# Performance work log

Hardware: AMD Instinct MI355X
Metric: run time of the kernel (lower is better)

The kernel has to match this reference:

```python
import jax, jax.numpy as jnp
import numpy as np

B, T_INIT, IN, H, OUT, GEN = 128, 50, 171, 1024, 171, 100


def setup_inputs() -> dict:
    key = jax.random.key(0)
    ks = jax.random.split(key, 20)
    s = 1.0 / np.sqrt(H)  # torch LSTMCell/Linear init scale

    def u(k, shape):
        return jax.random.uniform(k, shape, jnp.float32, -s, s)

    return {
        "initial_seq": jax.random.normal(ks[0], (B, T_INIT, IN), jnp.float32),
        "generate_frames_number": GEN,
        "w_ih1": u(ks[1], (4 * H, IN)), "w_hh1": u(ks[2], (4 * H, H)),
        "b_ih1": u(ks[3], (4 * H,)), "b_hh1": u(ks[4], (4 * H,)),
        "w_ih2": u(ks[5], (4 * H, H)), "w_hh2": u(ks[6], (4 * H, H)),
        "b_ih2": u(ks[7], (4 * H,)), "b_hh2": u(ks[8], (4 * H,)),
        "w_ih3": u(ks[9], (4 * H, H)), "w_hh3": u(ks[10], (4 * H, H)),
        "b_ih3": u(ks[11], (4 * H,)), "b_hh3": u(ks[12], (4 * H,)),
        "w_dec": u(ks[13], (OUT, H)), "b_dec": u(ks[14], (OUT,)),
    }


def _lstm_cell(x, h, c, w_ih, w_hh, b_ih, b_hh):
    # PyTorch LSTMCell: gates ordered (i, f, g, o)
    gates = x @ w_ih.T + b_ih + h @ w_hh.T + b_hh
    i, f, g, o = jnp.split(gates, 4, axis=-1)
    c_new = jax.nn.sigmoid(f) * c + jax.nn.sigmoid(i) * jnp.tanh(g)
    h_new = jax.nn.sigmoid(o) * jnp.tanh(c_new)
    return h_new, c_new


def reference(initial_seq, generate_frames_number,
              w_ih1, w_hh1, b_ih1, b_hh1,
              w_ih2, w_hh2, b_ih2, b_hh2,
              w_ih3, w_hh3, b_ih3, b_hh3,
              w_dec, b_dec):
    batch = initial_seq.shape[0]
    hid = w_hh1.shape[1]
    z = jnp.zeros((batch, hid), initial_seq.dtype)

    def step(carry, in_frame):
        h0, c0, h1, c1, h2, c2 = carry
        h0, c0 = _lstm_cell(in_frame, h0, c0, w_ih1, w_hh1, b_ih1, b_hh1)
        h1, c1 = _lstm_cell(h0, h1, c1, w_ih2, w_hh2, b_ih2, b_hh2)
        h2, c2 = _lstm_cell(h1, h2, c2, w_ih3, w_hh3, b_ih3, b_hh3)
        out = h2 @ w_dec.T + b_dec
        return (h0, c0, h1, c1, h2, c2), out

    # Conditioning phase: feed ground-truth frames; only states (and last out) matter.
    carry = (z, z, z, z, z, z)
    def cond_step(cs, frame):
        carry, _ = cs
        carry, out = step(carry, frame)
        return (carry, out), None
    (carry, current_frame), _ = jax.lax.scan(
        cond_step, (carry, jnp.zeros((batch, w_dec.shape[0]), initial_seq.dtype)),
        jnp.swapaxes(initial_seq, 0, 1))  # [T_init, B, IN]

    def gen_step(cs, _):
        carry, frame = cs
        carry, out = step(carry, frame)
        return (carry, out), out
    _, outs = jax.lax.scan(gen_step, (carry, current_frame), None,
                           length=generate_frames_number)
    return jnp.swapaxes(outs, 0, 1)  # [B, GEN, OUT]
```

## Files before the change

### kernel.cpp

```cpp
#include <hip/hip_runtime.h>

typedef __attribute__((ext_vector_type(8))) short short8;
typedef __attribute__((ext_vector_type(8))) _Float16 f16x8;
typedef __attribute__((ext_vector_type(4))) float f32x4;

#define GENF 100
#define TCOND 50
#define BATCH 128
#define HID 1024
#define INP 171
#define INPAD 192
#define OUTN 171
#define OUTPAD 176
#define SPLITS 4
#define TILES 64
#define PSTR ((size_t)BATCH * 4096)

static __device__ __forceinline__ unsigned short f2h(float f) {
  _Float16 h = (_Float16)f;
  return __builtin_bit_cast(unsigned short, h);
}
static __device__ __forceinline__ float h2f(unsigned short s) {
  return (float)__builtin_bit_cast(_Float16, s);
}
static __device__ __forceinline__ f16x8 ld8(const unsigned short* p) {
  short8 v = *reinterpret_cast<const short8*>(p);
  return __builtin_bit_cast(f16x8, v);
}
static __device__ __forceinline__ float sigm(float x) { return 1.f / (1.f + __expf(-x)); }

__global__ __launch_bounds__(256) void lstm_gemm_k(
    const unsigned short* __restrict__ xh_, const unsigned short* __restrict__ xl_,
    int ldx, int xc,
    const unsigned short* __restrict__ hh_, const unsigned short* __restrict__ hl_,
    const unsigned short* __restrict__ wP, int NKW, int nkr,
    const float* __restrict__ bias,
    float* __restrict__ c,
    unsigned short* __restrict__ ohh, unsigned short* __restrict__ ohl,
    unsigned short* __restrict__ histh, unsigned short* __restrict__ histl,
    float* __restrict__ partials, unsigned* __restrict__ counters, unsigned tgt)
{
  __shared__ __align__(16) char smem[98304];
  const int t = threadIdx.x;
  const int lane = t & 63, wv = t >> 6;
  const int nt = blockIdx.x & (TILES - 1), sp = blockIdx.x >> 6;
  const int n0 = nt * 64 + wv * 16;
  const int nit = NKW / SPLITS;
  const int beg = sp * nit;
  const int ns = nit >> 1;

  const int r_row = lane & 15, kg = lane >> 4;
  const int rslot = kg ^ (r_row & 3);
  const int srow = t >> 2;
  const unsigned short* wlane = wP + ((size_t)nt * NKW) * 2048
                                + (wv * 16 + r_row) * 32 + kg * 8;

  auto stage1 = [&](char* dst, int ck) {
    if (ck >= nkr) ck = 0;
    const unsigned short *sh, *sl;
    int ld, k0;
    if (ck < xc) { sh = xh_; sl = xl_; ld = ldx; k0 = ck * 32; }
    else { sh = hh_; sl = hl_; ld = HID; k0 = (ck - xc) * 32; }
#pragma unroll
    for (int j = 0; j < 2; ++j) {
      int rowp = j * 64 + srow;
      int slot = (t & 3) ^ (rowp & 3);
      const unsigned short* gh = sh + (size_t)rowp * ld + k0 + slot * 8;
      const unsigned short* gl = sl + (size_t)rowp * ld + k0 + slot * 8;
      char* dh = dst + j * 4096 + wv * 1024;
      char* dl = dst + 8192 + j * 4096 + wv * 1024;
      __builtin_amdgcn_global_load_lds((const __attribute__((address_space(1))) void*)gh,
                                       (__attribute__((address_space(3))) void*)dh, 16, 0, 0);
      __builtin_amdgcn_global_load_lds((const __attribute__((address_space(1))) void*)gl,
                                       (__attribute__((address_space(3))) void*)dl, 16, 0, 0);
    }
  };

  f32x4 zz = {0.f, 0.f, 0.f, 0.f};
  f32x4 acc[8] = {zz, zz, zz, zz, zz, zz, zz, zz};

  char* bA = smem;
  char* bB = smem + 32768;
  char* bC = smem + 65536;

  stage1(bA, beg);
  stage1(bA + 16384, beg + 1);
  f16x8 b0h0 = ld8(wlane + (size_t)(beg + 0) * 2048);
  f16x8 b0h1 = ld8(wlane + (size_t)(beg + 1) * 2048);
  __builtin_amdgcn_sched_barrier(0);
  stage1(bB, beg + 2);
  stage1(bB + 16384, beg + 3);
  f16x8 b1h0 = ld8(wlane + (size_t)(beg + 2) * 2048);
  f16x8 b1h1 = ld8(wlane + (size_t)(beg + 3) * 2048);
  __builtin_amdgcn_sched_barrier(0);

  for (int i = 0; i < ns; ++i) {
    int ck = beg + 2 * i + 4;
    if (ck >= beg + nit) ck = beg;
    stage1(bC, ck);
    stage1(bC + 16384, ck + 1);
    f16x8 b2h0 = ld8(wlane + (size_t)ck * 2048);
    f16x8 b2h1 = ld8(wlane + (size_t)(ck + 1) * 2048);
    __builtin_amdgcn_sched_barrier(0);

    asm volatile("s_waitcnt vmcnt(20)" ::: "memory");
    __builtin_amdgcn_s_barrier();
    __builtin_amdgcn_sched_barrier(0);

#pragma unroll
    for (int ch = 0; ch < 2; ++ch) {
      f16x8 ah[8], al[8];
#pragma unroll
      for (int rg = 0; rg < 8; ++rg) {
        int ro = ch * 16384 + (rg * 16 + r_row) * 64 + rslot * 16;
        ah[rg] = *reinterpret_cast<const f16x8*>(bA + ro);
        al[rg] = *reinterpret_cast<const f16x8*>(bA + ro + 8192);
      }
      f16x8 BH = ch ? b0h1 : b0h0;
#pragma unroll
      for (int rg = 0; rg < 8; ++rg)
        acc[rg] = __builtin_amdgcn_mfma_f32_16x16x32_f16(ah[rg], BH, acc[rg], 0, 0, 0);
#pragma unroll
      for (int rg = 0; rg < 8; ++rg)
        acc[rg] = __builtin_amdgcn_mfma_f32_16x16x32_f16(al[rg], BH, acc[rg], 0, 0, 0);
    }
    __builtin_amdgcn_sched_barrier(0);
    __builtin_amdgcn_s_barrier();

    char* tmp = bA; bA = bB; bB = bC; bC = tmp;
    b0h0 = b1h0; b0h1 = b1h1;
    b1h0 = b2h0; b1h1 = b2h1;
  }

  {
    float* pb = partials + (size_t)sp * PSTR;
    const int cn = n0 + r_row;
    const int mb = kg * 4;
#pragma unroll
    for (int rg = 0; rg < 8; ++rg)
#pragma unroll
      for (int r = 0; r < 4; ++r)
        pb[(size_t)(rg * 16 + mb + r) * 4096 + cn] = acc[rg][r];
  }

  __syncthreads();
  if (t == 0)
    __hip_atomic_fetch_add(&counters[nt], 1u, __ATOMIC_RELEASE, __HIP_MEMORY_SCOPE_AGENT);
  if (t == 0) {
    while (__hip_atomic_load(&counters[nt], __ATOMIC_RELAXED, __HIP_MEMORY_SCOPE_AGENT) < tgt)
      __builtin_amdgcn_s_sleep(2);
    (void)__hip_atomic_load(&counters[nt], __ATOMIC_ACQUIRE, __HIP_MEMORY_SCOPE_AGENT);
  }
  __syncthreads();

  const int fc = t & 15, fm = t >> 4;
  const int nh = nt * 16 + fc;
  const f32x4 bv = *reinterpret_cast<const f32x4*>(&bias[nh * 4]);
#pragma unroll
  for (int p = 0; p < 2; ++p) {
    int m = sp * 32 + p * 16 + fm;
    size_t gi0 = (size_t)m * 4096 + nh * 4;
    f32x4 s = *reinterpret_cast<const f32x4*>(&partials[gi0]);
#pragma unroll
    for (int q = 1; q < SPLITS; ++q)
      s += *reinterpret_cast<const f32x4*>(&partials[gi0 + (size_t)q * PSTR]);
    float gi = sigm(s[0] + bv[0]);
    float gf = sigm(s[1] + bv[1]);
    float gg = tanhf(s[2] + bv[2]);
    float go = sigm(s[3] + bv[3]);
    size_t sidx = (size_t)m * HID + nh;
    float cn2 = gf * c[sidx] + gi * gg;
    c[sidx] = cn2;
    float h = go * tanhf(cn2);
    unsigned short h16 = f2h(h);
    unsigned short l16 = f2h(h - h2f(h16));
    ohh[sidx] = h16;
    ohl[sidx] = l16;
    if (histh) { histh[sidx] = h16; histl[sidx] = l16; }
  }
}

__global__ __launch_bounds__(256) void decb_k(
    const unsigned short* __restrict__ histh, const unsigned short* __restrict__ histl,
    const unsigned short* __restrict__ wdh, const float* __restrict__ bd,
    float* __restrict__ outp)
{
  const int wave = threadIdx.x >> 6, lane = threadIdx.x & 63;
  const int n0 = ((int)blockIdx.x % 11) * 16;
  const int m0 = ((int)blockIdx.x / 11) * 16;
  const int row = lane & 15, kg = lane >> 4;
  f32x4 acc = {0.f, 0.f, 0.f, 0.f};
  const unsigned short* pah = histh + (size_t)(m0 + row) * HID + kg * 8 + wave * 256;
  const unsigned short* pal = histl + (size_t)(m0 + row) * HID + kg * 8 + wave * 256;
  const unsigned short* pbh = wdh + (size_t)(n0 + row) * HID + kg * 8 + wave * 256;
#pragma unroll
  for (int kk = 0; kk < 8; ++kk) {
    int off = kk * 32;
    f16x8 a1 = ld8(pah + off), a2 = ld8(pal + off);
    f16x8 b1 = ld8(pbh + off);
    acc = __builtin_amdgcn_mfma_f32_16x16x32_f16(a1, b1, acc, 0, 0, 0);
    acc = __builtin_amdgcn_mfma_f32_16x16x32_f16(a2, b1, acc, 0, 0, 0);
  }
  __shared__ f32x4 red[4][64];
  if (wave) red[wave][lane] = acc;
  __syncthreads();
  if (wave == 0) {
    acc += red[1][lane];
    acc += red[2][lane];
    acc += red[3][lane];
    const int col = lane & 15, rg = lane >> 4;
#pragma unroll
    for (int r = 0; r < 4; ++r) {
      int m = m0 + rg * 4 + r;
      int n = n0 + col;
      if (n < OUTN) {
        int tt = m >> 7, b = m & 127;
        outp[(size_t)b * (GENF * OUTN) + (size_t)tt * OUTN + n] = acc[r] + bd[n];
      }
    }
  }
}

__global__ void cvt_w_pack_k(const float* __restrict__ src, unsigned short* __restrict__ dst,
                             int C, int Cpad, int ck0, int NKW)
{
  int idx = blockIdx.x * 256 + threadIdx.x;
  if (idx >= 4096 * Cpad) return;
  int r = idx / Cpad, cc = idx - r * Cpad;
  float v = (cc < C) ? src[(size_t)r * C + cc] : 0.f;
  int rp = (r & 1023) * 4 + (r >> 10);
  int nt = rp >> 6, nc = rp & 63;
  int ck = ck0 + (cc >> 5), kk = cc & 31;
  dst[(((size_t)nt * NKW + ck) * 64 + nc) * 32 + kk] = f2h(v);
}

__global__ void cvt_plain_k(const float* __restrict__ src, unsigned short* __restrict__ w16,
                            int R, int C, int Rp, int Cp)
{
  int idx = blockIdx.x * 256 + threadIdx.x;
  if (idx >= Rp * Cp) return;
  int r = idx / Cp, c2 = idx - r * Cp;
  float v = (r < R && c2 < C) ? src[(size_t)r * C + c2] : 0.f;
  w16[idx] = f2h(v);
}

__global__ void cvt_wdt_k(const float* __restrict__ wdec, unsigned short* __restrict__ wdt)
{
  int idx = blockIdx.x * 256 + threadIdx.x;
  if (idx >= 1024 * 192) return;
  int k = idx / 192, j = idx - k * 192;
  float v = (j < OUTN) ? wdec[(size_t)j * HID + k] : 0.f;
  wdt[idx] = f2h(v);
}

__global__ __launch_bounds__(256) void weff_k(
    const unsigned short* __restrict__ wih, const unsigned short* __restrict__ wdt,
    unsigned short* __restrict__ W1g)
{
  const int wave = threadIdx.x >> 6, lane = threadIdx.x & 63;
  const int tile = blockIdx.x * 4 + wave;
  const int m0 = (tile >> 6) * 16;
  const int n0 = (tile & 63) * 16;
  const int row = lane & 15, kg = lane >> 4;
  f32x4 acc = {0.f, 0.f, 0.f, 0.f};
  const unsigned short* pa = wih + (size_t)(m0 + row) * 192 + kg * 8;
  const unsigned short* pb = wdt + (size_t)(n0 + row) * 192 + kg * 8;
#pragma unroll
  for (int kk = 0; kk < 6; ++kk) {
    int off = kk * 32;
    f16x8 a = ld8(pa + off);
    f16x8 b = ld8(pb + off);
    acc = __builtin_amdgcn_mfma_f32_16x16x32_f16(a, b, acc, 0, 0, 0);
  }
  const int col = lane & 15, rg = lane >> 4;
#pragma unroll
  for (int r = 0; r < 4; ++r) {
    int i = m0 + rg * 4 + r;
    int k2 = n0 + col;
    int rp = (i & 1023) * 4 + (i >> 10);
    int nt = rp >> 6, nc = rp & 63;
    int ck = k2 >> 5, kk2 = k2 & 31;
    W1g[(((size_t)nt * 64 + ck) * 64 + nc) * 32 + kk2] = f2h(acc[r]);
  }
}

__global__ void beff_k(const float* __restrict__ wih1, const float* __restrict__ bih,
                       const float* __restrict__ bhh, const float* __restrict__ bdec,
                       float* __restrict__ dst)
{
  int i = blockIdx.x * 256 + threadIdx.x;
  if (i >= 4096) return;
  float a = bih[i] + bhh[i];
  for (int j = 0; j < OUTN; ++j) a += wih1[(size_t)i * OUTN + j] * bdec[j];
  dst[(i & 1023) * 4 + (i >> 10)] = a;
}

__global__ void bias_perm_k(const float* __restrict__ a, const float* __restrict__ b,
                            float* __restrict__ dst)
{
  int i = blockIdx.x * 256 + threadIdx.x;
  if (i < 4096) dst[(i & 1023) * 4 + (i >> 10)] = a[i] + b[i];
}

__global__ void biaspad_k(const float* __restrict__ a, float* __restrict__ dst, int n, int np)
{
  int i = blockIdx.x * 256 + threadIdx.x;
  if (i < np) dst[i] = (i < n) ? a[i] : 0.f;
}

__global__ void xcond_k(const float* __restrict__ seq, unsigned short* __restrict__ xhi,
                        unsigned short* __restrict__ xlo)
{
  int idx = blockIdx.x * 256 + threadIdx.x;
  const int total = TCOND * BATCH * INPAD;
  if (idx >= total) return;
  int t = idx / (BATCH * INPAD);
  int rem = idx - t * (BATCH * INPAD);
  int b = rem / INPAD;
  int k = rem - b * INPAD;
  float v = (k < INP) ? seq[((size_t)b * TCOND + t) * INP + k] : 0.f;
  unsigned short h = f2h(v);
  xhi[idx] = h;
  xlo[idx] = f2h(v - h2f(h));
}

extern "C" void kernel_launch(void* const* d_in, const int* in_sizes, int n_in,
                              void* d_out, int out_size, void* d_ws, size_t ws_size,
                              hipStream_t stream)
{
  (void)in_sizes; (void)n_in; (void)out_size;
  const float* seq   = (const float*)d_in[0];
  const float* w_ih1 = (const float*)d_in[2];
  const float* w_hh1 = (const float*)d_in[3];
  const float* b_ih1 = (const float*)d_in[4];
  const float* b_hh1 = (const float*)d_in[5];
  const float* w_ih2 = (const float*)d_in[6];
  const float* w_hh2 = (const float*)d_in[7];
  const float* b_ih2 = (const float*)d_in[8];
  const float* b_hh2 = (const float*)d_in[9];
  const float* w_ih3 = (const float*)d_in[10];
  const float* w_hh3 = (const float*)d_in[11];
  const float* b_ih3 = (const float*)d_in[12];
  const float* b_hh3 = (const float*)d_in[13];
  const float* w_dec = (const float*)d_in[14];
  const float* b_dec = (const float*)d_in[15];
  float* out = (float*)d_out;

  char* ws = (char*)d_ws;
  size_t off = 0;
  auto alloc = [&](size_t bytes) -> char* {
    off = (off + 255) & ~(size_t)255;
    char* p = ws + off;
    off += bytes;
    return p;
  };
  auto us = [&](size_t n) { return (unsigned short*)alloc(n * 2); };
  auto fl = [&](size_t n) { return (float*)alloc(n * 4); };

  const int NK1C = 48;
  const int NK2 = 64;
  unsigned short* W1c = us((size_t)4096 * NK1C * 32);
  unsigned short* W1g = us((size_t)4096 * NK2 * 32);
  unsigned short* W2 = us((size_t)4096 * NK2 * 32);
  unsigned short* W3 = us((size_t)4096 * NK2 * 32);
  unsigned short* wd = us((size_t)OUTPAD * HID);
  unsigned short* wih1f = us((size_t)4096 * 192);
  unsigned short* wdt = us((size_t)1024 * 192);
  float *b1c = fl(4096), *beff = fl(4096), *b2 = fl(4096), *b3 = fl(4096), *bd = fl(OUTPAD);
  unsigned short *xch = us((size_t)TCOND * BATCH * INPAD), *xcl = us((size_t)TCOND * BATCH * INPAD);
  float* partials = fl((size_t)SPLITS * PSTR);
  unsigned short* histh = us((size_t)GENF * BATCH * HID);
  unsigned short* histl = us((size_t)GENF * BATCH * HID);

  size_t state_beg = (off + 255) & ~(size_t)255;
  float *c0 = fl((size_t)BATCH * HID), *c1 = fl((size_t)BATCH * HID), *c2 = fl((size_t)BATCH * HID);
  unsigned short* Hh[3][2];
  unsigned short* Hl[3][2];
  for (int L = 0; L < 3; ++L)
    for (int p = 0; p < 2; ++p) {
      Hh[L][p] = us((size_t)BATCH * HID);
      Hl[L][p] = us((size_t)BATCH * HID);
    }
  unsigned* counters = (unsigned*)alloc(3 * TILES * 4);
  size_t state_end = off;

  if (off > ws_size) return;

  hipMemsetAsync(ws + state_beg, 0, state_end - state_beg, stream);
  hipMemsetAsync(W1c, 0, (size_t)4096 * NK1C * 32 * 2, stream);

  cvt_w_pack_k<<<(4096 * INPAD + 255) / 256, 256, 0, stream>>>(w_ih1, W1c, INP, INPAD, 0, NK1C);
  cvt_w_pack_k<<<(4096 * 1024 + 255) / 256, 256, 0, stream>>>(w_hh1, W1c, HID, HID, 6, NK1C);
  cvt_w_pack_k<<<(4096 * 1024 + 255) / 256, 256, 0, stream>>>(w_hh1, W1g, HID, HID, 32, NK2);
  cvt_w_pack_k<<<(4096 * 1024 + 255) / 256, 256, 0, stream>>>(w_ih2, W2, HID, HID, 0, NK2);
  cvt_w_pack_k<<<(4096 * 1024 + 255) / 256, 256, 0, stream>>>(w_hh2, W2, HID, HID, 32, NK2);
  cvt_w_pack_k<<<(4096 * 1024 + 255) / 256, 256, 0, stream>>>(w_ih3, W3, HID, HID, 0, NK2);
  cvt_w_pack_k<<<(4096 * 1024 + 255) / 256, 256, 0, stream>>>(w_hh3, W3, HID, HID, 32, NK2);
  cvt_plain_k<<<(OUTPAD * HID + 255) / 256, 256, 0, stream>>>(w_dec, wd, OUTN, HID, OUTPAD, HID);
  cvt_plain_k<<<(4096 * 192 + 255) / 256, 256, 0, stream>>>(w_ih1, wih1f, 4096, INP, 4096, 192);
  cvt_wdt_k<<<(1024 * 192 + 255) / 256, 256, 0, stream>>>(w_dec, wdt);
  weff_k<<<4096, 256, 0, stream>>>(wih1f, wdt, W1g);
  beff_k<<<16, 256, 0, stream>>>(w_ih1, b_ih1, b_hh1, b_dec, beff);
  bias_perm_k<<<16, 256, 0, stream>>>(b_ih1, b_hh1, b1c);
  bias_perm_k<<<16, 256, 0, stream>>>(b_ih2, b_hh2, b2);
  bias_perm_k<<<16, 256, 0, stream>>>(b_ih3, b_hh3, b3);
  biaspad_k<<<1, 256, 0, stream>>>(b_dec, bd, OUTN, OUTPAD);
  xcond_k<<<(TCOND * BATCH * INPAD + 255) / 256, 256, 0, stream>>>(seq, xch, xcl);

  for (int s = 0; s < TCOND + GENF; ++s) {
    const int pp = s & 1, np = pp ^ 1;
    const unsigned tg = (unsigned)SPLITS * (unsigned)(s + 1);
    unsigned short *hsh = (unsigned short*)0, *hsl = (unsigned short*)0;
    if (s >= TCOND) {
      hsh = histh + (size_t)(s - TCOND) * BATCH * HID;
      hsl = histl + (size_t)(s - TCOND) * BATCH * HID;
    }
    if (s < TCOND) {
      lstm_gemm_k<<<TILES * SPLITS, 256, 0, stream>>>(
          xch + (size_t)s * BATCH * INPAD, xcl + (size_t)s * BATCH * INPAD, INPAD, 6,
          Hh[0][pp], Hl[0][pp], W1c, NK1C, 38, b1c, c0,
          Hh[0][np], Hl[0][np], (unsigned short*)0, (unsigned short*)0,
          partials, counters, tg);
    } else {
      lstm_gemm_k<<<TILES * SPLITS, 256, 0, stream>>>(
          Hh[2][pp], Hl[2][pp], HID, 32,
          Hh[0][pp], Hl[0][pp], W1g, NK2, NK2, beff, c0,
          Hh[0][np], Hl[0][np], (unsigned short*)0, (unsigned short*)0,
          partials, counters, tg);
    }
    lstm_gemm_k<<<TILES * SPLITS, 256, 0, stream>>>(
        Hh[0][np], Hl[0][np], HID, 32,
        Hh[1][pp], Hl[1][pp], W2, NK2, NK2, b2, c1,
        Hh[1][np], Hl[1][np], (unsigned short*)0, (unsigned short*)0,
        partials, counters + TILES, tg);
    lstm_gemm_k<<<TILES * SPLITS, 256, 0, stream>>>(
        Hh[1][np], Hl[1][np], HID, 32,
        Hh[2][pp], Hl[2][pp], W3, NK2, NK2, b3, c2,
        Hh[2][np], Hl[2][np], hsh, hsl,
        partials, counters + 2 * TILES, tg);
  }

  decb_k<<<(GENF * BATCH / 16) * 11, 256, 0, stream>>>(histh, histl, wd, bd, out);
}
```

Before: 12.56 ms.

## Widen GEMM N-tile to 128 columns and double K-splits per gate tile

Each block now computes 128 gate columns instead of 64 (two 16-column accumulator sets per wave), with tiles halved to 32 and K-splits doubled to 8. Each staged activation fragment in LDS is reused across twice as many MFMAs, halving activation reloads per block, and the weight packing is re-laid out to match. In exchange it uses more accumulator registers, writes more split-K partials, and has 8-way reduction traffic in the epilogue.

New measurement: 15.69 ms. +24.9%, slower.

```diff
diff --git a/kernel.cpp b/kernel.cpp
--- a/kernel.cpp
+++ b/kernel.cpp
@@ -12,8 +12,8 @@
 #define INPAD 192
 #define OUTN 171
 #define OUTPAD 176
-#define SPLITS 4
-#define TILES 64
+#define SPLITS 8
+#define TILES 32
 #define PSTR ((size_t)BATCH * 4096)
 
 static __device__ __forceinline__ unsigned short f2h(float f) {
@@ -43,8 +43,7 @@
   __shared__ __align__(16) char smem[98304];
   const int t = threadIdx.x;
   const int lane = t & 63, wv = t >> 6;
-  const int nt = blockIdx.x & (TILES - 1), sp = blockIdx.x >> 6;
-  const int n0 = nt * 64 + wv * 16;
+  const int nt = blockIdx.x & (TILES - 1), sp = blockIdx.x >> 5;
   const int nit = NKW / SPLITS;
   const int beg = sp * nit;
   const int ns = nit >> 1;
@@ -52,8 +51,8 @@
   const int r_row = lane & 15, kg = lane >> 4;
   const int rslot = kg ^ (r_row & 3);
   const int srow = t >> 2;
-  const unsigned short* wlane = wP + ((size_t)nt * NKW) * 2048
-                                + (wv * 16 + r_row) * 32 + kg * 8;
+  const unsigned short* wlane = wP + ((size_t)nt * NKW) * 4096
+                                + (wv * 32 + r_row) * 32 + kg * 8;
 
   auto stage1 = [&](char* dst, int ck) {
     if (ck >= nkr) ck = 0;
@@ -77,7 +76,8 @@
   };
 
   f32x4 zz = {0.f, 0.f, 0.f, 0.f};
-  f32x4 acc[8] = {zz, zz, zz, zz, zz, zz, zz, zz};
+  f32x4 acc0[8] = {zz, zz, zz, zz, zz, zz, zz, zz};
+  f32x4 acc1[8] = {zz, zz, zz, zz, zz, zz, zz, zz};
 
   char* bA = smem;
   char* bB = smem + 32768;
@@ -85,13 +85,17 @@
 
   stage1(bA, beg);
   stage1(bA + 16384, beg + 1);
-  f16x8 b0h0 = ld8(wlane + (size_t)(beg + 0) * 2048);
-  f16x8 b0h1 = ld8(wlane + (size_t)(beg + 1) * 2048);
+  f16x8 b0h0 = ld8(wlane + (size_t)(beg + 0) * 4096);
+  f16x8 b0g0 = ld8(wlane + (size_t)(beg + 0) * 4096 + 512);
+  f16x8 b0h1 = ld8(wlane + (size_t)(beg + 1) * 4096);
+  f16x8 b0g1 = ld8(wlane + (size_t)(beg + 1) * 4096 + 512);
   __builtin_amdgcn_sched_barrier(0);
   stage1(bB, beg + 2);
   stage1(bB + 16384, beg + 3);
-  f16x8 b1h0 = ld8(wlane + (size_t)(beg + 2) * 2048);
-  f16x8 b1h1 = ld8(wlane + (size_t)(beg + 3) * 2048);
+  f16x8 b1h0 = ld8(wlane + (size_t)(beg + 2) * 4096);
+  f16x8 b1g0 = ld8(wlane + (size_t)(beg + 2) * 4096 + 512);
+  f16x8 b1h1 = ld8(wlane + (size_t)(beg + 3) * 4096);
+  f16x8 b1g1 = ld8(wlane + (size_t)(beg + 3) * 4096 + 512);
   __builtin_amdgcn_sched_barrier(0);
 
   for (int i = 0; i < ns; ++i) {
@@ -99,11 +103,13 @@
     if (ck >= beg + nit) ck = beg;
     stage1(bC, ck);
     stage1(bC + 16384, ck + 1);
-    f16x8 b2h0 = ld8(wlane + (size_t)ck * 2048);
-    f16x8 b2h1 = ld8(wlane + (size_t)(ck + 1) * 2048);
+    f16x8 b2h0 = ld8(wlane + (size_t)ck * 4096);
+    f16x8 b2g0 = ld8(wlane + (size_t)ck * 4096 + 512);
+    f16x8 b2h1 = ld8(wlane + (size_t)(ck + 1) * 4096);
+    f16x8 b2g1 = ld8(wlane + (size_t)(ck + 1) * 4096 + 512);
     __builtin_amdgcn_sched_barrier(0);
 
-    asm volatile("s_waitcnt vmcnt(20)" ::: "memory");
+    asm volatile("s_waitcnt vmcnt(24)" ::: "memory");
     __builtin_amdgcn_s_barrier();
     __builtin_amdgcn_sched_barrier(0);
 
@@ -117,48 +123,56 @@
         al[rg] = *reinterpret_cast<const f16x8*>(bA + ro + 8192);
       }
       f16x8 BH = ch ? b0h1 : b0h0;
+      f16x8 BG = ch ? b0g1 : b0g0;
 #pragma unroll
       for (int rg = 0; rg < 8; ++rg)
-        acc[rg] = __builtin_amdgcn_mfma_f32_16x16x32_f16(ah[rg], BH, acc[rg], 0, 0, 0);
+        acc0[rg] = __builtin_amdgcn_mfma_f32_16x16x32_f16(ah[rg], BH, acc0[rg], 0, 0, 0);
 #pragma unroll
       for (int rg = 0; rg < 8; ++rg)
-        acc[rg] = __builtin_amdgcn_mfma_f32_16x16x32_f16(al[rg], BH, acc[rg], 0, 0, 0);
+        acc0[rg] = __builtin_amdgcn_mfma_f32_16x16x32_f16(al[rg], BH, acc0[rg], 0, 0, 0);
+#pragma unroll
+      for (int rg = 0; rg < 8; ++rg)
+        acc1[rg] = __builtin_amdgcn_mfma_f32_16x16x32_f16(ah[rg], BG, acc1[rg], 0, 0, 0);
+#pragma unroll
+      for (int rg = 0; rg < 8; ++rg)
+        acc1[rg] = __builtin_amdgcn_mfma_f32_16x16x32_f16(al[rg], BG, acc1[rg], 0, 0, 0);
     }
     __builtin_amdgcn_sched_barrier(0);
     __builtin_amdgcn_s_barrier();
 
     char* tmp = bA; bA = bB; bB = bC; bC = tmp;
-    b0h0 = b1h0; b0h1 = b1h1;
-    b1h0 = b2h0; b1h1 = b2h1;
+    b0h0 = b1h0; b0g0 = b1g0; b0h1 = b1h1; b0g1 = b1g1;
+    b1h0 = b2h0; b1g0 = b2g0; b1h1 = b2h1; b1g1 = b2g1;
   }
 
   {
     float* pb = partials + (size_t)sp * PSTR;
-    const int cn = n0 + r_row;
+    const int cn0 = nt * 128 + wv * 32 + r_row;
     const int mb = kg * 4;
 #pragma unroll
     for (int rg = 0; rg < 8; ++rg)
 #pragma unroll
-      for (int r = 0; r < 4; ++r)
-        pb[(size_t)(rg * 16 + mb + r) * 4096 + cn] = acc[rg][r];
+      for (int r = 0; r < 4; ++r) {
+        pb[(size_t)(rg * 16 + mb + r) * 4096 + cn0] = acc0[rg][r];
+        pb[(size_t)(rg * 16 + mb + r) * 4096 + cn0 + 16] = acc1[rg][r];
+      }
   }
 
   __syncthreads();
-  if (t == 0)
+  if (t == 0) {
     __hip_atomic_fetch_add(&counters[nt], 1u, __ATOMIC_RELEASE, __HIP_MEMORY_SCOPE_AGENT);
-  if (t == 0) {
     while (__hip_atomic_load(&counters[nt], __ATOMIC_RELAXED, __HIP_MEMORY_SCOPE_AGENT) < tgt)
       __builtin_amdgcn_s_sleep(2);
     (void)__hip_atomic_load(&counters[nt], __ATOMIC_ACQUIRE, __HIP_MEMORY_SCOPE_AGENT);
   }
   __syncthreads();
 
-  const int fc = t & 15, fm = t >> 4;
-  const int nh = nt * 16 + fc;
+  const int fc = t & 31, fm = t >> 5;
+  const int nh = nt * 32 + fc;
   const f32x4 bv = *reinterpret_cast<const f32x4*>(&bias[nh * 4]);
 #pragma unroll
   for (int p = 0; p < 2; ++p) {
-    int m = sp * 32 + p * 16 + fm;
+    int m = sp * 16 + p * 8 + fm;
     size_t gi0 = (size_t)m * 4096 + nh * 4;
     f32x4 s = *reinterpret_cast<const f32x4*>(&partials[gi0]);
 #pragma unroll
@@ -229,9 +243,9 @@
   int r = idx / Cpad, cc = idx - r * Cpad;
   float v = (cc < C) ? src[(size_t)r * C + cc] : 0.f;
   int rp = (r & 1023) * 4 + (r >> 10);
-  int nt = rp >> 6, nc = rp & 63;
+  int nt = rp >> 7, nc = rp & 127;
   int ck = ck0 + (cc >> 5), kk = cc & 31;
-  dst[(((size_t)nt * NKW + ck) * 64 + nc) * 32 + kk] = f2h(v);
+  dst[(((size_t)nt * NKW + ck) * 128 + nc) * 32 + kk] = f2h(v);
 }
 
 __global__ void cvt_plain_k(const float* __restrict__ src, unsigned short* __restrict__ w16,
@@ -278,9 +292,9 @@
     int i = m0 + rg * 4 + r;
     int k2 = n0 + col;
     int rp = (i & 1023) * 4 + (i >> 10);
-    int nt = rp >> 6, nc = rp & 63;
+    int nt = rp >> 7, nc = rp & 127;
     int ck = k2 >> 5, kk2 = k2 & 31;
-    W1g[(((size_t)nt * 64 + ck) * 64 + nc) * 32 + kk2] = f2h(acc[r]);
+    W1g[(((size_t)nt * 64 + ck) * 128 + nc) * 32 + kk2] = f2h(acc[r]);
   }
 }
 
```
